# Performance work log

Measured on AMD Instinct MI355X. Metric: run time of the kernel, lower is better.

## Reference

```python
import jax, jax.numpy as jnp
import numpy as np

B, S, NB = 8, 512, 23
INIT, E, R, T = 512, 256, 3, 2
NEG = -9e8

def _gru(x, h, wih, whh, bih, bhh):
    gi = x @ wih.T + bih
    gh = h @ whh.T + bhh
    ir, iz, inn = jnp.split(gi, 3, axis=-1)
    hr, hz, hn = jnp.split(gh, 3, axis=-1)
    r = jax.nn.sigmoid(ir + hr)
    z = jax.nn.sigmoid(iz + hz)
    n = jnp.tanh(inn + r * hn)
    return (1.0 - z) * n + z * h

def setup_inputs():
    key = jax.random.key(0)
    ks = jax.random.split(key, 30)
    def lin(k, o, i):
        return jax.random.normal(k, (o, i), jnp.float32) * 0.02
    def vec(k, n):
        return jax.random.normal(k, (n,), jnp.float32) * 0.02
    inp = {}
    inp["amino_list"] = jax.random.normal(ks[0], (B, S, INIT), jnp.float32)
    inp["amino_mask"] = (jax.random.uniform(ks[1], (B, S)) < 0.9).astype(jnp.float32)
    inp["emb_W"] = lin(ks[2], E, INIT); inp["emb_b"] = vec(ks[3], E)
    inp["nb_W"] = lin(ks[4], E, INIT); inp["nb_b"] = vec(ks[5], E)
    inp["align_W"] = jax.random.normal(ks[6], (R, 1, 2 * E), jnp.float32) * 0.02
    inp["align_b"] = jax.random.normal(ks[7], (R, 1), jnp.float32) * 0.02
    inp["attend_W"] = jax.random.normal(ks[8], (R, E, E), jnp.float32) * 0.02
    inp["attend_b"] = jax.random.normal(ks[9], (R, E), jnp.float32) * 0.02
    inp["gru_wih"] = jax.random.normal(ks[10], (R, 3 * E, E), jnp.float32) * 0.02
    inp["gru_whh"] = jax.random.normal(ks[11], (R, 3 * E, E), jnp.float32) * 0.02
    inp["gru_bih"] = jax.random.normal(ks[12], (R, 3 * E), jnp.float32) * 0.02
    inp["gru_bhh"] = jax.random.normal(ks[13], (R, 3 * E), jnp.float32) * 0.02
    inp["seq_align_W"] = lin(ks[14], 1, 2 * E); inp["seq_align_b"] = vec(ks[15], 1)
    inp["seq_attend_W"] = lin(ks[16], E, E); inp["seq_attend_b"] = vec(ks[17], E)
    inp["seq_gru_wih"] = lin(ks[18], 3 * E, E); inp["seq_gru_bih"] = vec(ks[19], 3 * E)
    inp["seq_gru_whh"] = lin(ks[20], 3 * E, E); inp["seq_gru_bhh"] = vec(ks[21], 3 * E)
    inp["amino_degree_list"] = jax.random.randint(ks[22], (B, S, NB), -1, S)
    return inp

def reference(amino_list, amino_mask, emb_W, emb_b, nb_W, nb_b, align_W, align_b,
              attend_W, attend_b, gru_wih, gru_whh, gru_bih, gru_bhh,
              seq_align_W, seq_align_b, seq_attend_W, seq_attend_b,
              seq_gru_wih, seq_gru_whh, seq_gru_bih, seq_gru_bhh, amino_degree_list):
    idx = amino_degree_list
    lrelu = jax.nn.leaky_relu
    # per-batch neighbor gather: (S,D),(S,NB) -> (S,NB,D); index -1 wraps (masked out below)
    gather = jax.vmap(lambda f, i: f[i])
    feat = lrelu(amino_list @ emb_W.T + emb_b)               # (B,S,E)
    nfeat = lrelu(gather(amino_list, idx) @ nb_W.T + nb_b)   # (B,S,NB,E)
    attend_mask = (idx != -1).astype(feat.dtype)             # (B,S,NB)
    smask = jnp.where(idx == -1, NEG, 0.0).astype(feat.dtype)

    def attn(d, center, nbr):
        # align Linear on concat([center, nbr]) split into two matvecs (same math, no concat)
        aW = align_W[d, 0]
        score = lrelu(jnp.einsum('bse,e->bs', center, aW[:E])[:, :, None]
                      + jnp.einsum('bsne,e->bsn', nbr, aW[E:]) + align_b[d, 0])
        w = jax.nn.softmax(score + smask, axis=-1) * attend_mask   # softmax over neighbor axis
        nt = nbr @ attend_W[d].T + attend_b[d]
        return jax.nn.elu(jnp.einsum('bsn,bsne->bse', w, nt))

    h = _gru(attn(0, feat, nfeat).reshape(-1, E), feat.reshape(-1, E),
             gru_wih[0], gru_whh[0], gru_bih[0], gru_bhh[0])
    act = jax.nn.relu(h.reshape(B, S, E))
    for d in range(1, R):
        ctx = attn(d, act, gather(act, idx))
        h = _gru(ctx.reshape(-1, E), h, gru_wih[d], gru_whh[d], gru_bih[d], gru_bhh[d])
        act = jax.nn.relu(h.reshape(B, S, E))

    seq_feature = jnp.sum(act * amino_mask[:, :, None], axis=1)  # (B,E)
    act_mol = jax.nn.relu(seq_feature)                           # fixed across T (as in torch)
    seq_smask = jnp.where(amino_mask == 0, NEG, 0.0)
    saW = seq_align_W[0]
    act_seq = act_mol
    for _ in range(T):
        score = lrelu((act_mol @ saW[:E])[:, None]
                      + jnp.einsum('bse,e->bs', act, saW[E:]) + seq_align_b[0])
        w = jax.nn.softmax(score + seq_smask, axis=-1) * amino_mask  # softmax over seq axis
        tf = act @ seq_attend_W.T + seq_attend_b
        seq_ctx = jax.nn.elu(jnp.einsum('bs,bse->be', w, tf))
        seq_feature = _gru(seq_ctx, seq_feature, seq_gru_wih, seq_gru_whh, seq_gru_bih, seq_gru_bhh)
        act_seq = jax.nn.relu(seq_feature)
    return (act_seq, act)
```

## Files before the change

### kernel.cpp

```cpp
#include <hip/hip_runtime.h>
#include <math.h>


#define BSZ   8
#define SEQ   512
#define NBR   23
#define EMB   256
#define INITD 512
#define BS    (BSZ*SEQ)
#define G3    (3*EMB)
#define NEGV  -9e8f

typedef __attribute__((ext_vector_type(8))) short short8;
typedef __attribute__((ext_vector_type(4))) float f32x4;

__device__ __forceinline__ float lrelu(float x){ return x > 0.f ? x : 0.01f*x; }
__device__ __forceinline__ float elu1 (float x){ return x > 0.f ? x : (expf(x)-1.f); }
__device__ __forceinline__ float sigm (float x){ return 1.f/(1.f+expf(-x)); }
__device__ __forceinline__ float bf2f(ushort u){
    union { unsigned int i; float f; } v; v.i = ((unsigned int)u) << 16; return v.f;
}
__device__ __forceinline__ ushort f2bf(float f){
    union { float f; unsigned int i; } v; v.f = f;
    unsigned int u = v.i;
    return (ushort)((u + 0x7FFFu + ((u >> 16) & 1u)) >> 16);
}
__device__ __forceinline__ unsigned pk2(float a, float b){
    return (unsigned)f2bf(a) | ((unsigned)f2bf(b) << 16);
}
__device__ __forceinline__ void unpack8(uint4 v, float* o) {
    o[0]=bf2f((ushort)(v.x&0xffff)); o[1]=bf2f((ushort)(v.x>>16));
    o[2]=bf2f((ushort)(v.y&0xffff)); o[3]=bf2f((ushort)(v.y>>16));
    o[4]=bf2f((ushort)(v.z&0xffff)); o[5]=bf2f((ushort)(v.z>>16));
    o[6]=bf2f((ushort)(v.w&0xffff)); o[7]=bf2f((ushort)(v.w>>16));
}

__device__ __forceinline__ void gload_lds16(const void* g, void* l) {
    __builtin_amdgcn_global_load_lds(
        (const __attribute__((address_space(1))) unsigned int*)g,
        (__attribute__((address_space(3))) unsigned int*)l,
        16, 0, 0);
}

__device__ __forceinline__ void conv_unit(const float* s, ushort* d, size_t i) {
    float4 a = *reinterpret_cast<const float4*>(s + i);
    float4 b = *reinterpret_cast<const float4*>(s + i + 4);
    uint4 o;
    o.x = pk2(a.x, a.y); o.y = pk2(a.z, a.w);
    o.z = pk2(b.x, b.y); o.w = pk2(b.z, b.w);
    *reinterpret_cast<uint4*>(d + i) = o;
}

__global__ __launch_bounds__(256) void convert_core(
    const float* __restrict__ amino, ushort* __restrict__ aminobf,
    const float* __restrict__ embW,  ushort* __restrict__ embWbf,
    const float* __restrict__ nbW,   ushort* __restrict__ nbWbf,
    float* __restrict__ zeroBase)
{
    const unsigned stride = gridDim.x * 256;
    for (unsigned u = blockIdx.x*256 + threadIdx.x; u < 296192u; u += stride) {
        if      (u < 262144u) conv_unit(amino, aminobf, (size_t)u*8);
        else if (u < 278528u) conv_unit(embW,  embWbf,  (size_t)(u-262144u)*8);
        else if (u < 294912u) conv_unit(nbW,   nbWbf,   (size_t)(u-278528u)*8);
        else {
            unsigned i = (u - 294912u) * 8;
            *reinterpret_cast<float4*>(&zeroBase[i])     = make_float4(0,0,0,0);
            *reinterpret_cast<float4*>(&zeroBase[i + 4]) = make_float4(0,0,0,0);
        }
    }
}

__device__ __forceinline__ void convert_rest(
    int blk, int nblk,
    const float* attW, ushort* attWbf,
    const float* gwih, ushort* gwihbf,
    const float* gwhh, ushort* gwhhbf,
    const float* satW, ushort* satWbf,
    const float* sgwih, ushort* sgwihbf,
    const float* sgwhh, ushort* sgwhhbf)
{
    const unsigned stride = nblk * 256;
    for (unsigned u = blk*256 + threadIdx.x; u < 229376u; u += stride) {
        if      (u < 24576u)  conv_unit(attW,  attWbf,  (size_t)u*8);
        else if (u < 98304u)  conv_unit(gwih,  gwihbf,  (size_t)(u-24576u)*8);
        else if (u < 172032u) conv_unit(gwhh,  gwhhbf,  (size_t)(u-98304u)*8);
        else if (u < 180224u) conv_unit(satW,  satWbf,  (size_t)(u-172032u)*8);
        else if (u < 204800u) conv_unit(sgwih, sgwihbf, (size_t)(u-180224u)*8);
        else                  conv_unit(sgwhh, sgwhhbf, (size_t)(u-204800u)*8);
    }
}

struct GemmLds64 { ushort A[2][128][64]; ushort B[2][64][64]; };

template<int ACT, int DOTS>
__device__ __forceinline__ void gemm64_dev(
    const ushort* __restrict__ A, const ushort* __restrict__ W,
    const float* __restrict__ bias,
    float* __restrict__ C, ushort* __restrict__ Cbf,
    const float* __restrict__ dotW, float* __restrict__ dotOut,
    int N, int K, int bx, int by, GemmLds64& L)
{
    const int tid = threadIdx.x;
    const int m0 = bx * 128, n0 = by * 64;
    const int wv = tid >> 6, lane = tid & 63;
    const int fr = lane & 15, grp = lane >> 4;
    const int kc = K >> 3;
    const int mh = wv & 1, nh = wv >> 1;
    const int lrow = lane >> 3;
    const int csrc = (lane & 7) ^ lrow;

    f32x4 acc[4][2];
    #pragma unroll
    for (int i = 0; i < 4; ++i)
        #pragma unroll
        for (int n = 0; n < 2; ++n) acc[i][n] = (f32x4){0.f,0.f,0.f,0.f};

    auto stage = [&](int c, int k0) {
        const int kch = (k0 >> 3) + csrc;
        #pragma unroll
        for (int i = 0; i < 4; ++i) {
            const int s = (wv << 2) + i;
            gload_lds16(A + ((size_t)(m0 + (s << 3) + lrow) * kc + kch) * 8,
                        &L.A[c][s << 3][0]);
        }
        #pragma unroll
        for (int i = 0; i < 2; ++i) {
            const int s = (wv << 1) + i;
            gload_lds16(W + ((size_t)(n0 + (s << 3) + lrow) * kc + kch) * 8,
                        &L.B[c][s << 3][0]);
        }
    };
    auto compute = [&](int c) {
        #pragma unroll
        for (int ks = 0; ks < 2; ++ks) {
            short8 af[4];
            #pragma unroll
            for (int i = 0; i < 4; ++i) {
                const int ar = (mh << 6) + (i << 4) + fr;
                af[i] = *reinterpret_cast<const short8*>(
                    &L.A[c][ar][(((ks << 2) + grp) ^ (ar & 7)) << 3]);
            }
            #pragma unroll
            for (int n = 0; n < 2; ++n) {
                const int br = (nh << 5) + (n << 4) + fr;
                short8 bv = *reinterpret_cast<const short8*>(
                    &L.B[c][br][(((ks << 2) + grp) ^ (br & 7)) << 3]);
                #pragma unroll
                for (int i = 0; i < 4; ++i)
                    acc[i][n] = __builtin_amdgcn_mfma_f32_16x16x32_bf16(
                        af[i], bv, acc[i][n], 0, 0, 0);
            }
        }
    };

    const int KT = K >> 6;
    stage(0, 0);
    __syncthreads();
    int cur = 0;
    for (int kt = 1; kt < KT; ++kt) {
        stage(cur ^ 1, kt << 6);
        compute(cur);
        __syncthreads();
        cur ^= 1;
    }
    compute(cur);

    float pd[4][4];
    if (DOTS) {
        #pragma unroll
        for (int i = 0; i < 4; ++i)
            #pragma unroll
            for (int j = 0; j < 4; ++j) pd[i][j] = 0.f;
    }
    #pragma unroll
    for (int i = 0; i < 4; ++i) {
        const int mrow = m0 + (mh << 6) + (i << 4) + (grp << 2);
        #pragma unroll
        for (int n = 0; n < 2; ++n) {
            const int col = n0 + (nh << 5) + (n << 4) + fr;
            const float bv = bias[col];
            const float dw = DOTS ? dotW[col] : 0.f;
            #pragma unroll
            for (int j = 0; j < 4; ++j) {
                float t = acc[i][n][j] + bv;
                if (ACT == 1) t = lrelu(t);
                size_t off = (size_t)(mrow + j) * N + col;
                if (C)   C[off] = t;
                if (Cbf) Cbf[off] = f2bf(t);
                if (DOTS) pd[i][j] += t * dw;
            }
        }
    }
    if (DOTS) {
        #pragma unroll
        for (int i = 0; i < 4; ++i)
            #pragma unroll
            for (int j = 0; j < 4; ++j) {
                float v = pd[i][j];
                v += __shfl_xor(v, 1, 64);
                v += __shfl_xor(v, 2, 64);
                v += __shfl_xor(v, 4, 64);
                v += __shfl_xor(v, 8, 64);
                if (fr == 0)
                    atomicAdd(&dotOut[m0 + (mh << 6) + (i << 4) + (grp << 2) + j], v);
            }
    }
}

__global__ __launch_bounds__(256) void featnbase_kernel(
    const ushort* __restrict__ aminobf,
    const ushort* __restrict__ embWbf, const float* __restrict__ embB,
    ushort* __restrict__ featbf,
    const ushort* __restrict__ nbWbf, const float* __restrict__ nbB,
    ushort* __restrict__ nbasebf,
    const float* __restrict__ alignW,
    float* __restrict__ cdot, float* __restrict__ ndot,
    const float* attW, ushort* attWbf,
    const float* gwih, ushort* gwihbf,
    const float* gwhh, ushort* gwhhbf,
    const float* satW, ushort* satWbf,
    const float* sgwih, ushort* sgwihbf,
    const float* sgwhh, ushort* sgwhhbf)
{
    __shared__ GemmLds64 L;
    int blk = blockIdx.x;
    if (blk < 128)
        gemm64_dev<1,1>(aminobf, embWbf, embB, nullptr, featbf,
                        alignW, cdot, EMB, INITD, blk & 31, blk >> 5, L);
    else if (blk < 256) {
        blk -= 128;
        gemm64_dev<1,1>(aminobf, nbWbf, nbB, nullptr, nbasebf,
                        alignW + EMB, ndot, EMB, INITD, blk & 31, blk >> 5, L);
    } else {
        convert_rest(blk - 256, 128, attW, attWbf, gwih, gwihbf,
                     gwhh, gwhhbf, satW, satWbf, sgwih, sgwihbf, sgwhh, sgwhhbf);
    }
}

struct GALds { ushort ctxpre[16][256]; ushort ctx[16][256]; float wsum_s[16]; };

__global__ __launch_bounds__(512) void gatherattend_kernel(
    const float* __restrict__ cdot, const float* __restrict__ ndot,
    const int* __restrict__ idx, const ushort* __restrict__ nbr,
    const float* __restrict__ alignBd,
    const ushort* __restrict__ attWd, const float* __restrict__ attBd,
    ushort* __restrict__ ctxbf)
{
    __shared__ GALds L;
    const int tid = threadIdx.x;
    const int r0 = blockIdx.x * 16;

    {
        const int row16 = tid >> 5, sub = tid & 31;
        const int r = r0 + row16, b = r >> 9;
        float sc = -3e38f, vm = 0.f; int rn = 0;
        if (sub < NBR) {
            int j = idx[(size_t)r*NBR + sub];
            int valid = (j >= 0);
            int jj = valid ? j : j + SEQ;
            rn = b*SEQ + jj;
            vm = (float)valid;
            sc = lrelu(cdot[r] + ndot[rn] + alignBd[0]) + (valid ? 0.f : NEGV);
        }
        float m = sc;
        #pragma unroll
        for (int off = 16; off; off >>= 1) m = fmaxf(m, __shfl_xor(m, off, 32));
        float ev = (sub < NBR) ? expf(sc - m) : 0.f;
        float s = ev;
        #pragma unroll
        for (int off = 16; off; off >>= 1) s += __shfl_xor(s, off, 32);
        float wgt = ev * vm / s;
        float ws = wgt;
        #pragma unroll
        for (int off = 16; off; off >>= 1) ws += __shfl_xor(ws, off, 32);
        float a8[8] = {};
        const int e0 = sub << 3;
        #pragma unroll
        for (int n = 0; n < NBR; ++n) {
            float wn = __shfl(wgt, n, 32);
            int   rr = __shfl(rn, n, 32);
            uint4 v = *reinterpret_cast<const uint4*>(&nbr[(size_t)rr*EMB + e0]);
            float x[8]; unpack8(v, x);
            #pragma unroll
            for (int i = 0; i < 8; ++i) a8[i] += wn * x[i];
        }
        uint4 o;
        o.x = pk2(a8[0],a8[1]); o.y = pk2(a8[2],a8[3]);
        o.z = pk2(a8[4],a8[5]); o.w = pk2(a8[6],a8[7]);
        *reinterpret_cast<uint4*>(&L.ctxpre[row16][(sub ^ (row16&7)) << 3]) = o;
        if (sub == 0) L.wsum_s[row16] = ws;
    }
    __syncthreads();

    const int wv = tid >> 6, lane = tid & 63;
    const int fr = lane & 15, grp = lane >> 4;
    {
        f32x4 acc[2] = {(f32x4){0,0,0,0},(f32x4){0,0,0,0}};
        #pragma unroll
        for (int kt = 0; kt < 8; ++kt) {
            short8 af = *reinterpret_cast<const short8*>(
                &L.ctxpre[fr][((((kt<<2)+grp) ^ (fr&7)) << 3)]);
            #pragma unroll
            for (int f = 0; f < 2; ++f) {
                const int col = (wv<<5) + (f<<4) + fr;
                short8 bv = *reinterpret_cast<const short8*>(
                    &attWd[(size_t)col*EMB + (kt<<5) + (grp<<3)]);
                acc[f] = __builtin_amdgcn_mfma_f32_16x16x32_bf16(af, bv, acc[f], 0, 0, 0);
            }
        }
        #pragma unroll
        for (int f = 0; f < 2; ++f) {
            const int col = (wv<<5) + (f<<4) + fr;
            const float bb = attBd[col];
            #pragma unroll
            for (int j = 0; j < 4; ++j) {
                const int row = (grp<<2) + j;
                L.ctx[row][col] = f2bf(elu1(acc[f][j] + L.wsum_s[row]*bb));
            }
        }
    }
    __syncthreads();
    {
        const int row = tid >> 5, c = tid & 31;
        uint4 v = *reinterpret_cast<const uint4*>(&L.ctx[row][c << 3]);
        *reinterpret_cast<uint4*>(&ctxbf[(size_t)(r0+row)*EMB + (c << 3)]) = v;
    }
}

__global__ __launch_bounds__(256) void gigh_kernel(
    const ushort* __restrict__ ctxbf, const ushort* __restrict__ gwihd,
    const float* __restrict__ gbihd, ushort* __restrict__ gibf,
    const ushort* __restrict__ hprevbf, const ushort* __restrict__ gwhhd,
    const float* __restrict__ gbhhd, ushort* __restrict__ ghbf)
{
    __shared__ GemmLds64 L;
    int blk = blockIdx.x;
    if (blk < 384)
        gemm64_dev<0,0>(ctxbf, gwihd, gbihd, nullptr, gibf, nullptr, nullptr,
                        G3, EMB, blk & 31, blk >> 5, L);
    else {
        blk -= 384;
        gemm64_dev<0,0>(hprevbf, gwhhd, gbhhd, nullptr, ghbf, nullptr, nullptr,
                        G3, EMB, blk & 31, blk >> 5, L);
    }
}

template<int LAST>
__global__ __launch_bounds__(512) void grudot_kernel(
    const ushort* __restrict__ gibf, const ushort* __restrict__ ghbf,
    const ushort* __restrict__ hprevbf, const float* __restrict__ nextW,
    const float* __restrict__ mask,
    ushort* __restrict__ hbf, float* __restrict__ actout,
    ushort* __restrict__ actbf,
    float* __restrict__ cdotO, float* __restrict__ ndotO,
    float* __restrict__ seqfeatA)
{
    __shared__ float sred[16][256];
    const int tid = threadIdx.x;
    const int row = tid >> 5, sub = tid & 31;
    const int e0 = sub << 3;
    const size_t r = (size_t)blockIdx.x * 16 + row;
    const size_t gb = r*G3;
    uint4 giA = *reinterpret_cast<const uint4*>(&gibf[gb + e0]);
    uint4 giB = *reinterpret_cast<const uint4*>(&gibf[gb + 256 + e0]);
    uint4 giC = *reinterpret_cast<const uint4*>(&gibf[gb + 512 + e0]);
    uint4 ghA = *reinterpret_cast<const uint4*>(&ghbf[gb + e0]);
    uint4 ghB = *reinterpret_cast<const uint4*>(&ghbf[gb + 256 + e0]);
    uint4 ghC = *reinterpret_cast<const uint4*>(&ghbf[gb + 512 + e0]);
    uint4 hpv = *reinterpret_cast<const uint4*>(&hprevbf[r*EMB + e0]);
    float ir_[8], iz_[8], in_[8], hr_[8], hz_[8], hn_[8], hp_[8];
    unpack8(giA, ir_); unpack8(giB, iz_); unpack8(giC, in_);
    unpack8(ghA, hr_); unpack8(ghB, hz_); unpack8(ghC, hn_);
    unpack8(hpv, hp_);
    float hv8[8], av8[8];
    #pragma unroll
    for (int i = 0; i < 8; ++i) {
        float rg = sigm(ir_[i] + hr_[i]);
        float z  = sigm(iz_[i] + hz_[i]);
        float n  = tanhf(in_[i] + rg*hn_[i]);
        hv8[i] = (1.f - z)*n + z*hp_[i];
        av8[i] = fmaxf(hv8[i], 0.f);
    }
    if (LAST) {
        *reinterpret_cast<float4*>(&actout[r*EMB + e0])     = make_float4(av8[0],av8[1],av8[2],av8[3]);
        *reinterpret_cast<float4*>(&actout[r*EMB + e0 + 4]) = make_float4(av8[4],av8[5],av8[6],av8[7]);
    }
    uint4 hb, ab;
    hb.x = pk2(hv8[0],hv8[1]); hb.y = pk2(hv8[2],hv8[3]);
    hb.z = pk2(hv8[4],hv8[5]); hb.w = pk2(hv8[6],hv8[7]);
    ab.x = pk2(av8[0],av8[1]); ab.y = pk2(av8[2],av8[3]);
    ab.z = pk2(av8[4],av8[5]); ab.w = pk2(av8[6],av8[7]);
    *reinterpret_cast<uint4*>(&hbf[r*EMB + e0])   = hb;
    *reinterpret_cast<uint4*>(&actbf[r*EMB + e0]) = ab;
    float pc = 0.f, pn = 0.f;
    float4 w1a = *reinterpret_cast<const float4*>(&nextW[EMB + e0]);
    float4 w1b = *reinterpret_cast<const float4*>(&nextW[EMB + e0 + 4]);
    pn = av8[0]*w1a.x + av8[1]*w1a.y + av8[2]*w1a.z + av8[3]*w1a.w
       + av8[4]*w1b.x + av8[5]*w1b.y + av8[6]*w1b.z + av8[7]*w1b.w;
    if (!LAST) {
        float4 w0a = *reinterpret_cast<const float4*>(&nextW[e0]);
        float4 w0b = *reinterpret_cast<const float4*>(&nextW[e0 + 4]);
        pc = av8[0]*w0a.x + av8[1]*w0a.y + av8[2]*w0a.z + av8[3]*w0a.w
           + av8[4]*w0b.x + av8[5]*w0b.y + av8[6]*w0b.z + av8[7]*w0b.w;
    }
    #pragma unroll
    for (int off = 16; off; off >>= 1) {
        pn += __shfl_xor(pn, off, 32);
        if (!LAST) pc += __shfl_xor(pc, off, 32);
    }
    if (sub == 0) {
        if (!LAST) cdotO[r] = pc;
        ndotO[r] = pn;
    }
    if (LAST) {
        const float mk = mask[r];
        #pragma unroll
        for (int i = 0; i < 8; ++i) sred[row][e0 + i] = av8[i] * mk;
        __syncthreads();
        if (tid < 256) {
            float s = 0.f;
            #pragma unroll
            for (int rr = 0; rr < 16; ++rr) s += sred[rr][tid];
            atomicAdd(&seqfeatA[(blockIdx.x >> 5)*EMB + tid], s);
        }
    }
}

__global__ __launch_bounds__(256) void seqpvtf_kernel(
    const float* __restrict__ ad, const float* __restrict__ mask,
    const float* __restrict__ saB, const float* __restrict__ saW,
    const float* __restrict__ seqfeat,
    const ushort* __restrict__ actbf, const ushort* __restrict__ satWbf,
    const float* __restrict__ satB,
    float* __restrict__ partial)
{
    const int st = blockIdx.x, b = blockIdx.y;
    const int tid = threadIdx.x;
    __shared__ ushort As[32][256];
    __shared__ float tf_s[32][256];
    __shared__ float w_s[SEQ];
    __shared__ float red[256];
    const int r0 = b*SEQ + st*32;

    {
        #pragma unroll
        for (int i = 0; i < 4; ++i) {
            const int row = (tid >> 5) + i*8, c = tid & 31;
            uint4 v = *reinterpret_cast<const uint4*>(&actbf[(size_t)(r0+row)*EMB + (c<<3)]);
            *reinterpret_cast<uint4*>(&As[row][(c ^ (row&7)) << 3]) = v;
        }
    }
    red[tid] = fmaxf(seqfeat[b*EMB + tid], 0.f) * saW[tid];
    __syncthreads();
    for (int off = 128; off; off >>= 1) {
        if (tid < off) red[tid] += red[tid + off];
        __syncthreads();
    }
    const float cb = red[0];
    __syncthreads();
    float mk0 = mask[b*SEQ + tid], mk1 = mask[b*SEQ + 256 + tid];
    float bb = saB[0];
    float s0 = lrelu(cb + ad[b*SEQ + tid] + bb)       + (mk0 == 0.f ? NEGV : 0.f);
    float s1 = lrelu(cb + ad[b*SEQ + 256 + tid] + bb) + (mk1 == 0.f ? NEGV : 0.f);
    red[tid] = fmaxf(s0, s1); __syncthreads();
    for (int off = 128; off; off >>= 1) {
        if (tid < off) red[tid] = fmaxf(red[tid], red[tid + off]);
        __syncthreads();
    }
    float m = red[0]; __syncthreads();
    float e0v = expf(s0 - m), e1v = expf(s1 - m);
    red[tid] = e0v + e1v; __syncthreads();
    for (int off = 128; off; off >>= 1) {
        if (tid < off) red[tid] += red[tid + off];
        __syncthreads();
    }
    float inv = 1.f / red[0];
    w_s[tid]       = e0v * inv * mk0;
    w_s[tid + 256] = e1v * inv * mk1;
    __syncthreads();

    {
        const int wv = tid >> 6, lane = tid & 63;
        const int fr = lane & 15, grp = lane >> 4;
        f32x4 acc[2][4];
        #pragma unroll
        for (int mt = 0; mt < 2; ++mt)
            #pragma unroll
            for (int f = 0; f < 4; ++f) acc[mt][f] = (f32x4){0,0,0,0};
        #pragma unroll
        for (int kt = 0; kt < 8; ++kt) {
            short8 af[2];
            #pragma unroll
            for (int mt = 0; mt < 2; ++mt) {
                const int ar = (mt << 4) + fr;
                af[mt] = *reinterpret_cast<const short8*>(
                    &As[ar][((((kt<<2)+grp) ^ (ar&7)) << 3)]);
            }
            #pragma unroll
            for (int f = 0; f < 4; ++f) {
                const int col = (wv<<6) + (f<<4) + fr;
                short8 bv = *reinterpret_cast<const short8*>(
                    &satWbf[(size_t)col*EMB + (kt<<5) + (grp<<3)]);
                #pragma unroll
                for (int mt = 0; mt < 2; ++mt)
                    acc[mt][f] = __builtin_amdgcn_mfma_f32_16x16x32_bf16(
                        af[mt], bv, acc[mt][f], 0, 0, 0);
            }
        }
        #pragma unroll
        for (int f = 0; f < 4; ++f) {
            const int col = (wv<<6) + (f<<4) + fr;
            const float bias = satB[col];
            #pragma unroll
            for (int mt = 0; mt < 2; ++mt)
                #pragma unroll
                for (int j = 0; j < 4; ++j)
                    tf_s[(mt<<4) + (grp<<2) + j][col] = acc[mt][f][j] + bias;
        }
    }
    __syncthreads();
    {
        float acc = 0.f;
        const int s0i = st * 32;
        #pragma unroll 4
        for (int s = 0; s < 32; ++s)
            acc += w_s[s0i + s] * tf_s[s][tid];
        partial[((size_t)b*16 + st)*EMB + tid] = acc;
    }
}

template<int T0>
__global__ __launch_bounds__(512) void seqstep_kernel(
    const float* __restrict__ partial, const float* __restrict__ sfin,
    const ushort* __restrict__ sgwihbf, const float* __restrict__ sgbih,
    const ushort* __restrict__ sgwhhbf, const float* __restrict__ sgbhh,
    float* __restrict__ sgi, float* __restrict__ sfout,
    float* __restrict__ actseq)
{
    const int b = blockIdx.x >> 2, q = blockIdx.x & 3;
    const int tid = threadIdx.x, lane = tid & 63, wv = tid >> 6;
    __shared__ float xs[EMB];
    __shared__ float hs[EMB];
    __shared__ float gis[192], ghs[192];
    if (tid < EMB) {
        hs[tid] = sfin[b*EMB + tid];
        if (T0) {
            float a = 0.f;
            #pragma unroll
            for (int st = 0; st < 16; ++st)
                a += partial[((size_t)b*16 + st)*EMB + tid];
            xs[tid] = elu1(a);
        }
    }
    if (!T0) {
        for (int l = tid; l < 192; l += 512) {
            int g = (l >> 6)*EMB + (q << 6) + (l & 63);
            gis[l] = sgi[b*G3 + g];
        }
    }
    __syncthreads();
    const int nrows = T0 ? 384 : 192;
    const int rpw = nrows >> 3;
    for (int i = 0; i < rpw; ++i) {
        const int l = wv * rpw + i;
        const int iswih = T0 && (l < 192);
        const int ll = (T0 && l >= 192) ? l - 192 : l;
        const int g = (ll >> 6)*EMB + (q << 6) + (ll & 63);
        const ushort* Wm = iswih ? sgwihbf : sgwhhbf;
        ushort4 w4 = *reinterpret_cast<const ushort4*>(&Wm[(size_t)g*EMB + (lane << 2)]);
        float4 x4 = *reinterpret_cast<const float4*>(iswih ? &xs[lane << 2] : &hs[lane << 2]);
        float d = bf2f(w4.x)*x4.x + bf2f(w4.y)*x4.y + bf2f(w4.z)*x4.z + bf2f(w4.w)*x4.w;
        #pragma unroll
        for (int off = 32; off; off >>= 1) d += __shfl_xor(d, off, 64);
        if (lane == 0) {
            if (iswih) {
                d += sgbih[g];
                gis[ll] = d;
                sgi[b*G3 + g] = d;
            } else {
                ghs[ll] = d + sgbhh[g];
            }
        }
    }
    __syncthreads();
    if (tid < 64) {
        const int e = (q << 6) + tid;
        float rg = sigm(gis[tid]       + ghs[tid]);
        float z  = sigm(gis[64 + tid]  + ghs[64 + tid]);
        float n  = tanhf(gis[128 + tid] + rg*ghs[128 + tid]);
        float hv = (1.f - z)*n + z*hs[e];
        sfout[b*EMB + e]  = hv;
        actseq[b*EMB + e] = fmaxf(hv, 0.f);
    }
}

extern "C" void kernel_launch(void* const* d_in, const int* in_sizes, int n_in,
                              void* d_out, int out_size, void* d_ws, size_t ws_size,
                              hipStream_t stream) {
    (void)in_sizes; (void)n_in; (void)out_size; (void)ws_size;
    const float* amino  = (const float*)d_in[0];
    const float* mask   = (const float*)d_in[1];
    const float* embW   = (const float*)d_in[2];
    const float* embB   = (const float*)d_in[3];
    const float* nbW    = (const float*)d_in[4];
    const float* nbB    = (const float*)d_in[5];
    const float* alignW = (const float*)d_in[6];
    const float* alignB = (const float*)d_in[7];
    const float* attW   = (const float*)d_in[8];
    const float* attB   = (const float*)d_in[9];
    const float* gwih   = (const float*)d_in[10];
    const float* gwhh   = (const float*)d_in[11];
    const float* gbih   = (const float*)d_in[12];
    const float* gbhh   = (const float*)d_in[13];
    const float* saW    = (const float*)d_in[14];
    const float* saB    = (const float*)d_in[15];
    const float* satW   = (const float*)d_in[16];
    const float* satB   = (const float*)d_in[17];
    const float* sgwih  = (const float*)d_in[18];
    const float* sgbih  = (const float*)d_in[19];
    const float* sgwhh  = (const float*)d_in[20];
    const float* sgbhh  = (const float*)d_in[21];
    const int*   idx    = (const int*)d_in[22];

    char* cur = (char*)d_ws;
    auto alloc = [&](size_t bytes) -> char* {
        char* p = cur; cur += (bytes + 255) & ~(size_t)255; return p;
    };
    float* seqfeat = (float*)alloc(BSZ*EMB*4);
    float* cdot    = (float*)alloc(BS*4);
    float* ndot    = (float*)alloc(BS*4);
    float* sf2     = (float*)alloc(BSZ*EMB*4);
    float* sgi     = (float*)alloc(BSZ*G3*4);
    float* partial = (float*)alloc((size_t)BSZ*16*EMB*4);
    ushort* aminobf  = (ushort*)alloc((size_t)BS*INITD*2);
    ushort* featbf   = (ushort*)alloc((size_t)BS*EMB*2);
    ushort* nbasebf  = (ushort*)alloc((size_t)BS*EMB*2);
    ushort* actbf    = (ushort*)alloc((size_t)BS*EMB*2);
    ushort* hbf      = (ushort*)alloc((size_t)BS*EMB*2);
    ushort* ctxbf    = (ushort*)alloc((size_t)BS*EMB*2);
    ushort* gibf     = (ushort*)alloc((size_t)BS*G3*2);
    ushort* ghbf     = (ushort*)alloc((size_t)BS*G3*2);
    ushort* embWbf   = (ushort*)alloc((size_t)EMB*INITD*2);
    ushort* nbWbf    = (ushort*)alloc((size_t)EMB*INITD*2);
    ushort* attWbf   = (ushort*)alloc((size_t)3*EMB*EMB*2);
    ushort* gwihbf   = (ushort*)alloc((size_t)3*G3*EMB*2);
    ushort* gwhhbf   = (ushort*)alloc((size_t)3*G3*EMB*2);
    ushort* satWbf   = (ushort*)alloc((size_t)EMB*EMB*2);
    ushort* sgwihbf  = (ushort*)alloc((size_t)G3*EMB*2);
    ushort* sgwhhbf  = (ushort*)alloc((size_t)G3*EMB*2);

    float* out    = (float*)d_out;
    float* actseq = out;
    float* act    = out + BSZ*EMB;

    convert_core<<<1280, 256, 0, stream>>>(
        amino, aminobf, embW, embWbf, nbW, nbWbf, seqfeat);

    featnbase_kernel<<<384, 256, 0, stream>>>(
        aminobf, embWbf, embB, featbf, nbWbf, nbB, nbasebf,
        alignW, cdot, ndot,
        attW, attWbf, gwih, gwihbf, gwhh, gwhhbf,
        satW, satWbf, sgwih, sgwihbf, sgwhh, sgwhhbf);

    for (int d = 0; d < 3; ++d) {
        const ushort* nbrbf   = (d == 0) ? nbasebf : actbf;
        const ushort* hprevbf = (d == 0) ? featbf  : hbf;
        gatherattend_kernel<<<BS/16, 512, 0, stream>>>(
            cdot, ndot, idx, nbrbf, alignB + d,
            attWbf + (size_t)d*EMB*EMB, attB + d*EMB, ctxbf);
        gigh_kernel<<<768, 256, 0, stream>>>(
            ctxbf, gwihbf + (size_t)d*G3*EMB, gbih + d*G3, gibf,
            hprevbf, gwhhbf + (size_t)d*G3*EMB, gbhh + d*G3, ghbf);
        if (d < 2) {
            grudot_kernel<0><<<BS/16, 512, 0, stream>>>(
                gibf, ghbf, hprevbf, alignW + (d+1)*2*EMB, mask,
                hbf, act, actbf, cdot, ndot, seqfeat);
        } else {
            grudot_kernel<1><<<BS/16, 512, 0, stream>>>(
                gibf, ghbf, hprevbf, saW, mask,
                hbf, act, actbf, cdot, ndot, seqfeat);
        }
    }

    seqpvtf_kernel<<<dim3(16, BSZ), 256, 0, stream>>>(
        ndot, mask, saB, saW, seqfeat, actbf, satWbf, satB, partial);
    seqstep_kernel<1><<<32, 512, 0, stream>>>(
        partial, seqfeat, sgwihbf, sgbih, sgwhhbf, sgbhh, sgi, sf2, actseq);
    seqstep_kernel<0><<<32, 512, 0, stream>>>(
        partial, sf2, sgwihbf, sgbih, sgwhhbf, sgbhh, sgi, seqfeat, actseq);
}
```

Measured before the change: 157.0 us.

## Co-schedule gather-attend with hidden-state GEMM and use 128x128 GEMM tiles

The gh = h·Whh GEMM does not depend on the attention context, so it now runs in the same launch as the gather-attend blocks, sharing LDS through a union. The gi GEMM becomes its own launch that runs after the context is ready. Both GEMMs move to a new 128x128-tile double-buffered MFMA routine with 512 threads in place of the 64-tile version. This is meant to overlap independent work, reduce launch count per round, and raise data reuse per tile. The trade-off is larger LDS use per block, which may lower occupancy, and fewer blocks (192) for the gi GEMM.

```diff
diff --git a/kernel.cpp b/kernel.cpp
--- a/kernel.cpp
+++ b/kernel.cpp
@@ -204,6 +204,92 @@
                 if (fr == 0)
                     atomicAdd(&dotOut[m0 + (mh << 6) + (i << 4) + (grp << 2) + j], v);
             }
+    }
+}
+
+struct GemmLds128 { ushort A[2][128][64]; ushort B[2][128][64]; };
+
+__device__ __forceinline__ void gemm128_dev(
+    const ushort* __restrict__ A, const ushort* __restrict__ W,
+    const float* __restrict__ bias, ushort* __restrict__ Cbf,
+    int N, int K, int bx, int by, GemmLds128& L)
+{
+    const int tid = threadIdx.x;
+    const int m0 = bx * 128, n0 = by * 128;
+    const int wv = tid >> 6, lane = tid & 63;
+    const int fr = lane & 15, grp = lane >> 4;
+    const int kc = K >> 3;
+    const int mh = wv & 1, nq = wv >> 1;
+    const int lrow = lane >> 3;
+    const int csrc = (lane & 7) ^ lrow;
+
+    f32x4 acc[4][2];
+    #pragma unroll
+    for (int i = 0; i < 4; ++i)
+        #pragma unroll
+        for (int n = 0; n < 2; ++n) acc[i][n] = (f32x4){0.f,0.f,0.f,0.f};
+
+    auto stage = [&](int c, int k0) {
+        const int kch = (k0 >> 3) + csrc;
+        #pragma unroll
+        for (int i = 0; i < 2; ++i) {
+            const int s = (wv << 1) + i;
+            gload_lds16(A + ((size_t)(m0 + (s << 3) + lrow) * kc + kch) * 8,
+                        &L.A[c][s << 3][0]);
+        }
+        #pragma unroll
+        for (int i = 0; i < 2; ++i) {
+            const int s = (wv << 1) + i;
+            gload_lds16(W + ((size_t)(n0 + (s << 3) + lrow) * kc + kch) * 8,
+                        &L.B[c][s << 3][0]);
+        }
+    };
+    auto compute = [&](int c) {
+        #pragma unroll
+        for (int ks = 0; ks < 2; ++ks) {
+            short8 af[4];
+            #pragma unroll
+            for (int i = 0; i < 4; ++i) {
+                const int ar = (mh << 6) + (i << 4) + fr;
+                af[i] = *reinterpret_cast<const short8*>(
+                    &L.A[c][ar][(((ks << 2) + grp) ^ (ar & 7)) << 3]);
+            }
+            #pragma unroll
+            for (int n = 0; n < 2; ++n) {
+                const int br = (nq << 5) + (n << 4) + fr;
+                short8 bv = *reinterpret_cast<const short8*>(
+                    &L.B[c][br][(((ks << 2) + grp) ^ (br & 7)) << 3]);
+                #pragma unroll
+                for (int i = 0; i < 4; ++i)
+                    acc[i][n] = __builtin_amdgcn_mfma_f32_16x16x32_bf16(
+                        af[i], bv, acc[i][n], 0, 0, 0);
+            }
+        }
+    };
+
+    const int KT = K >> 6;
+    stage(0, 0);
+    __syncthreads();
+    int cur = 0;
+    for (int kt = 1; kt < KT; ++kt) {
+        stage(cur ^ 1, kt << 6);
+        compute(cur);
+        __syncthreads();
+        cur ^= 1;
+    }
+    compute(cur);
+
+    #pragma unroll
+    for (int i = 0; i < 4; ++i) {
+        const int mrow = m0 + (mh << 6) + (i << 4) + (grp << 2);
+        #pragma unroll
+        for (int n = 0; n < 2; ++n) {
+            const int col = n0 + (nq << 5) + (n << 4) + fr;
+            const float bv = bias[col];
+            #pragma unroll
+            for (int j = 0; j < 4; ++j)
+                Cbf[(size_t)(mrow + j) * N + col] = f2bf(acc[i][n][j] + bv);
+        }
     }
 }
 
@@ -238,17 +324,18 @@
 }
 
 struct GALds { ushort ctxpre[16][256]; ushort ctx[16][256]; float wsum_s[16]; };
-
-__global__ __launch_bounds__(512) void gatherattend_kernel(
+union RoundLds { GALds ga; GemmLds128 g; };
+
+__device__ __forceinline__ void gatherattend_dev(
+    int blk,
     const float* __restrict__ cdot, const float* __restrict__ ndot,
     const int* __restrict__ idx, const ushort* __restrict__ nbr,
     const float* __restrict__ alignBd,
     const ushort* __restrict__ attWd, const float* __restrict__ attBd,
-    ushort* __restrict__ ctxbf)
-{
-    __shared__ GALds L;
+    ushort* __restrict__ ctxbf, GALds& L)
+{
     const int tid = threadIdx.x;
-    const int r0 = blockIdx.x * 16;
+    const int r0 = blk * 16;
 
     {
         const int row16 = tid >> 5, sub = tid & 31;
@@ -327,22 +414,33 @@
     }
 }
 
-__global__ __launch_bounds__(256) void gigh_kernel(
-    const ushort* __restrict__ ctxbf, const ushort* __restrict__ gwihd,
-    const float* __restrict__ gbihd, ushort* __restrict__ gibf,
+__global__ __launch_bounds__(512) void gagh2_kernel(
+    const float* __restrict__ cdot, const float* __restrict__ ndot,
+    const int* __restrict__ idx, const ushort* __restrict__ nbr,
+    const float* __restrict__ alignBd,
+    const ushort* __restrict__ attWd, const float* __restrict__ attBd,
+    ushort* __restrict__ ctxbf,
     const ushort* __restrict__ hprevbf, const ushort* __restrict__ gwhhd,
     const float* __restrict__ gbhhd, ushort* __restrict__ ghbf)
 {
-    __shared__ GemmLds64 L;
-    int blk = blockIdx.x;
-    if (blk < 384)
-        gemm64_dev<0,0>(ctxbf, gwihd, gbihd, nullptr, gibf, nullptr, nullptr,
-                        G3, EMB, blk & 31, blk >> 5, L);
-    else {
-        blk -= 384;
-        gemm64_dev<0,0>(hprevbf, gwhhd, gbhhd, nullptr, ghbf, nullptr, nullptr,
-                        G3, EMB, blk & 31, blk >> 5, L);
-    }
+    __shared__ RoundLds L;
+    if (blockIdx.x < 256) {
+        gatherattend_dev(blockIdx.x, cdot, ndot, idx, nbr, alignBd,
+                         attWd, attBd, ctxbf, L.ga);
+    } else {
+        int blk = blockIdx.x - 256;
+        gemm128_dev(hprevbf, gwhhd, gbhhd, ghbf, G3, EMB,
+                    blk & 31, blk >> 5, L.g);
+    }
+}
+
+__global__ __launch_bounds__(512) void gi_kernel(
+    const ushort* __restrict__ ctxbf, const ushort* __restrict__ gwihd,
+    const float* __restrict__ gbihd, ushort* __restrict__ gibf)
+{
+    __shared__ GemmLds128 L;
+    gemm128_dev(ctxbf, gwihd, gbihd, gibf, G3, EMB,
+                blockIdx.x & 31, blockIdx.x >> 5, L);
 }
 
 template<int LAST>
@@ -665,12 +763,12 @@
     for (int d = 0; d < 3; ++d) {
         const ushort* nbrbf   = (d == 0) ? nbasebf : actbf;
         const ushort* hprevbf = (d == 0) ? featbf  : hbf;
-        gatherattend_kernel<<<BS/16, 512, 0, stream>>>(
+        gagh2_kernel<<<448, 512, 0, stream>>>(
             cdot, ndot, idx, nbrbf, alignB + d,
-            attWbf + (size_t)d*EMB*EMB, attB + d*EMB, ctxbf);
-        gigh_kernel<<<768, 256, 0, stream>>>(
-            ctxbf, gwihbf + (size_t)d*G3*EMB, gbih + d*G3, gibf,
+            attWbf + (size_t)d*EMB*EMB, attB + d*EMB, ctxbf,
             hprevbf, gwhhbf + (size_t)d*G3*EMB, gbhh + d*G3, ghbf);
+        gi_kernel<<<192, 512, 0, stream>>>(
+            ctxbf, gwihbf + (size_t)d*G3*EMB, gbih + d*G3, gibf);
         if (d < 2) {
             grudot_kernel<0><<<BS/16, 512, 0, stream>>>(
                 gibf, ghbf, hprevbf, alignW + (d+1)*2*EMB, mask,
```

Measured after the change: 165.7 us. 5.6% more time.
